# Performance work log

Measured on AMD Instinct MI355X. Metric: run time of the kernel, lower is better.

## Reference

```python
import jax, jax.numpy as jnp
import numpy as np

D = 1024
H = 16
HD = D // H


def setup_inputs() -> dict:
    key = jax.random.key(0)
    ks = jax.random.split(key, 5)
    s = 1.0 / np.sqrt(D)
    return {
        "inputs": jax.random.normal(ks[0], (2, 2048, D), dtype=jnp.float32),
        "Wq": jax.random.normal(ks[1], (D, D), dtype=jnp.float32) * s,
        "bq": jnp.zeros((D,), jnp.float32),
        "Wk": jax.random.normal(ks[2], (D, D), dtype=jnp.float32) * s,
        "bk": jnp.zeros((D,), jnp.float32),
        "Wv": jax.random.normal(ks[3], (D, D), dtype=jnp.float32) * s,
        "bv": jnp.zeros((D,), jnp.float32),
        "Wo": jax.random.normal(ks[4], (D, D), dtype=jnp.float32) * s,
        "bo": jnp.zeros((D,), jnp.float32),
    }


def reference(inputs, Wq, bq, Wk, bk, Wv, bv, Wo, bo):
    B, S, _ = inputs.shape
    def split_heads(x):  # [B,S,D] -> [B,H,S,hd]
        return x.reshape(B, S, H, HD).transpose(0, 2, 1, 3)
    q = split_heads(inputs @ Wq + bq)
    k = split_heads(inputs @ Wk + bk)
    v = split_heads(inputs @ Wv + bv)
    scale = 1.0 / jnp.sqrt(jnp.asarray(HD, inputs.dtype))
    scores = jnp.einsum("bhsd,bhtd->bhst", q, k) * scale  # [B,H,S,S]
    weights = jax.nn.softmax(scores, axis=-1)
    attn = jnp.einsum("bhst,bhtd->bhsd", weights, v)
    concat = attn.transpose(0, 2, 1, 3).reshape(B, S, D)
    return concat @ Wo + bo
```

## Files before the change

kernel.cpp:

```cpp
#include <hip/hip_runtime.h>


typedef __bf16 bf16x8 __attribute__((ext_vector_type(8)));
typedef float  f32x4  __attribute__((ext_vector_type(4)));

#if __has_builtin(__builtin_amdgcn_exp2f)
#define EXPFN(x) __builtin_amdgcn_exp2f(x)
#define QSCALE (0.125f * 1.44269504088896f)
#else
#define EXPFN(x) __expf(x)
#define QSCALE 0.125f
#endif

#define LDKP 74

__device__ __forceinline__ unsigned short f2bf(float f) {
    unsigned int u = __float_as_uint(f);
    u += 0x7FFFu + ((u >> 16) & 1u);
    return (unsigned short)(u >> 16);
}

__device__ __forceinline__ void gload16(const void* g, void* l) {
    __builtin_amdgcn_global_load_lds(
        (const __attribute__((address_space(1))) void*)g,
        (__attribute__((address_space(3))) void*)l, 16, 0, 0);
}

#define WAIT0_BARRIER() asm volatile("s_waitcnt vmcnt(0)\n\ts_barrier" ::: "memory")

__global__ __launch_bounds__(256) void prep_kernel(
    const float* __restrict__ X, ushort4* __restrict__ Xb,
    const float* __restrict__ Wq, const float* __restrict__ Wk,
    const float* __restrict__ Wv, const float* __restrict__ Wo,
    unsigned short* __restrict__ Wt_all) {
    const int z = blockIdx.z;
    if (z == 4) {
        int base = (blockIdx.y * 32 + blockIdx.x) * 1024 + threadIdx.x;
        const float4* X4 = (const float4*)X;
        #pragma unroll
        for (int c = 0; c < 4; c++) {
            int i = base + c * 256;
            float4 v = X4[i];
            ushort4 o;
            o.x = f2bf(v.x); o.y = f2bf(v.y); o.z = f2bf(v.z); o.w = f2bf(v.w);
            Xb[i] = o;
        }
        return;
    }
    __shared__ float tile[32][33];
    const float* W = (z == 0) ? Wq : (z == 1) ? Wk : (z == 2) ? Wv : Wo;
    unsigned short* Wt = Wt_all + (size_t)z * 1024 * 1024;
    int c0 = blockIdx.x * 32, r0 = blockIdx.y * 32;
    int x = threadIdx.x & 31, y = threadIdx.x >> 5;
    for (int j = 0; j < 32; j += 8)
        tile[y + j][x] = W[(r0 + y + j) * 1024 + c0 + x];
    __syncthreads();
    for (int j = 0; j < 32; j += 8)
        Wt[(c0 + y + j) * 1024 + r0 + x] = f2bf(tile[x][y + j]);
}

__global__ __launch_bounds__(256, 2) void gemm_qkv_kernel(
    const unsigned short* __restrict__ Xb, const unsigned short* __restrict__ Wt_all,
    const float* __restrict__ bq, const float* __restrict__ bk,
    const float* __restrict__ bv,
    unsigned short* __restrict__ Qb, unsigned short* __restrict__ Kb,
    unsigned short* __restrict__ Vt) {
    const int x0 = blockIdx.x * 128;
    const int y0 = blockIdx.y * 64;

    __shared__ __align__(16) unsigned short smem[128 * 64 + 3 * 64 * 64];
    unsigned short* As  = smem;
    unsigned short* Bqs = smem + 8192;
    unsigned short* Bks = smem + 12288;
    unsigned short* Bvs = smem + 16384;

    const unsigned short* Ap  = Xb + (size_t)x0 * 1024;
    const unsigned short* Bqp = Wt_all + (size_t)y0 * 1024;
    const unsigned short* Bkp = Wt_all + 1048576u + (size_t)y0 * 1024;
    const unsigned short* Bvp = Wt_all + 2097152u + (size_t)y0 * 1024;

    const int tid = threadIdx.x;
    const int lane = tid & 63, wave = tid >> 6;
    const int quad = lane >> 4, l15 = lane & 15;
    const int wrow = (wave >> 1) * 64, wcol = (wave & 1) * 32;

    f32x4 aq[4][2] = {};
    f32x4 ak[4][2] = {};
    f32x4 av[4][2] = {};

    const int srow = lane >> 3;
    const int ch8  = (lane & 7) * 8;
    const int swz  = (((lane & 7) ^ srow)) * 8;
    const int sw   = (l15 & 7);

    for (int k0 = 0; k0 < 1024; k0 += 64) {
        #pragma unroll
        for (int c = 0; c < 4; c++) {
            int r = c * 32 + wave * 8 + srow;
            gload16(Ap + (size_t)r * 1024 + k0 + swz, &As[r * 64 + ch8]);
        }
        #pragma unroll
        for (int c = 0; c < 2; c++) {
            int r = c * 32 + wave * 8 + srow;
            gload16(Bqp + (size_t)r * 1024 + k0 + swz, &Bqs[r * 64 + ch8]);
            gload16(Bkp + (size_t)r * 1024 + k0 + swz, &Bks[r * 64 + ch8]);
            gload16(Bvp + (size_t)r * 1024 + k0 + swz, &Bvs[r * 64 + ch8]);
        }
        WAIT0_BARRIER();
        #pragma unroll
        for (int kk = 0; kk < 2; kk++) {
            bf16x8 af[4], bqf[2], bkf[2], bvf[2];
            const int co = (((kk * 4 + quad) ^ sw)) * 8;
            #pragma unroll
            for (int i = 0; i < 4; i++)
                af[i] = *(const bf16x8*)&As[(wrow + i * 16 + l15) * 64 + co];
            #pragma unroll
            for (int j = 0; j < 2; j++) {
                bqf[j] = *(const bf16x8*)&Bqs[(wcol + j * 16 + l15) * 64 + co];
                bkf[j] = *(const bf16x8*)&Bks[(wcol + j * 16 + l15) * 64 + co];
                bvf[j] = *(const bf16x8*)&Bvs[(wcol + j * 16 + l15) * 64 + co];
            }
            #pragma unroll
            for (int i = 0; i < 4; i++)
                #pragma unroll
                for (int j = 0; j < 2; j++) {
                    aq[i][j] = __builtin_amdgcn_mfma_f32_16x16x32_bf16(
                        af[i], bqf[j], aq[i][j], 0, 0, 0);
                    ak[i][j] = __builtin_amdgcn_mfma_f32_16x16x32_bf16(
                        af[i], bkf[j], ak[i][j], 0, 0, 0);
                    av[i][j] = __builtin_amdgcn_mfma_f32_16x16x32_bf16(
                        af[i], bvf[j], av[i][j], 0, 0, 0);
                }
        }
        __syncthreads();
    }

    #pragma unroll
    for (int j = 0; j < 2; j++) {
        int col = y0 + wcol + j * 16 + l15;
        float bqc = bq[col], bkc = bk[col];
        int h = col >> 6, d = col & 63;
        #pragma unroll
        for (int i = 0; i < 4; i++)
            #pragma unroll
            for (int r = 0; r < 4; r++) {
                int row = x0 + wrow + i * 16 + quad * 4 + r;
                int b = row >> 11, s = row & 2047;
                size_t idx = (size_t)((b * 16 + h) * 2048 + s) * 64 + d;
                Qb[idx] = f2bf((aq[i][j][r] + bqc) * QSCALE);
                Kb[idx] = f2bf(ak[i][j][r] + bkc);
            }
    }

    __syncthreads();
    unsigned short* vts = smem;
    #pragma unroll
    for (int j = 0; j < 2; j++) {
        int n = wcol + j * 16 + l15;
        float bvc = bv[y0 + n];
        #pragma unroll
        for (int i = 0; i < 4; i++)
            #pragma unroll
            for (int r = 0; r < 4; r++) {
                int m = wrow + i * 16 + quad * 4 + r;
                vts[n * 136 + m] = f2bf(av[i][j][r] + bvc);
            }
    }
    __syncthreads();
    const int bseq = x0 >> 11;
    const int s0 = x0 & 2047;
    #pragma unroll
    for (int q = 0; q < 4; q++) {
        int c = q * 256 + tid;
        int n = c >> 4, mc = c & 15;
        uint4 vv = *(const uint4*)&vts[n * 136 + mc * 8];
        *(uint4*)&Vt[(size_t)(bseq * 1024 + y0 + n) * 2048 + s0 + mc * 8] = vv;
    }
}

__global__ __launch_bounds__(256) void attn_kernel(
    const unsigned short* __restrict__ Qb, const unsigned short* __restrict__ Kb,
    const unsigned short* __restrict__ Vt, unsigned short* __restrict__ Cc,
    float* __restrict__ Op, float* __restrict__ Lp, int tlen, int do_split) {
    const int bh = blockIdx.y;
    const int b = bh >> 4, h = bh & 15;
    const int q0 = blockIdx.x * 128;
    const int split = blockIdx.z;
    const int tbeg = split * tlen;

    const int tid = threadIdx.x;
    const int lane = tid & 63, wave = tid >> 6;
    const int quad = lane >> 4, l15 = lane & 15;

    __shared__ __align__(16) unsigned short Ks[64 * 64];
    __shared__ __align__(16) unsigned short Vs[64 * 64];
    __shared__ __align__(16) unsigned short Ps[4][32 * LDKP];

    const unsigned short* Qbh = Qb + (size_t)bh * 2048 * 64;
    const unsigned short* Kbh = Kb + (size_t)bh * 2048 * 64;
    const unsigned short* Vbh = Vt + (size_t)bh * 64 * 2048;

    bf16x8 qa[2][2];
    #pragma unroll
    for (int mi = 0; mi < 2; mi++)
        #pragma unroll
        for (int kk = 0; kk < 2; kk++)
            qa[mi][kk] = *(const bf16x8*)&Qbh[
                (size_t)(q0 + wave * 32 + mi * 16 + l15) * 64 + kk * 32 + quad * 8];

    union { unsigned short us[8]; bf16x8 v; } ones_u;
    #pragma unroll
    for (int i = 0; i < 8; i++) ones_u.us[i] = 0x3F80;
    const bf16x8 onesv = ones_u.v;

    f32x4 o[2][4] = {};
    f32x4 ol[2] = {};

    const int srow = lane >> 3;
    const int r0s = wave * 16 + srow;
    const int ch8 = (lane & 7) * 8;
    const int swz = (((lane & 7) ^ srow)) * 8;
    const int sw  = (l15 & 7);

    for (int ti = 0; ti < tlen; ti += 64) {
        const int t0 = tbeg + ti;
        __syncthreads();
        gload16(&Kbh[(size_t)(t0 + r0s) * 64 + swz],       &Ks[r0s * 64 + ch8]);
        gload16(&Kbh[(size_t)(t0 + r0s + 8) * 64 + swz],   &Ks[(r0s + 8) * 64 + ch8]);
        gload16(&Vbh[(size_t)r0s * 2048 + t0 + swz],       &Vs[r0s * 64 + ch8]);
        gload16(&Vbh[(size_t)(r0s + 8) * 2048 + t0 + swz], &Vs[(r0s + 8) * 64 + ch8]);
        asm volatile("s_waitcnt vmcnt(0)" ::: "memory");
        __syncthreads();

        f32x4 sf[2][4] = {};
        #pragma unroll
        for (int j = 0; j < 4; j++)
            #pragma unroll
            for (int kk = 0; kk < 2; kk++) {
                bf16x8 kf = *(const bf16x8*)&Ks[(j * 16 + l15) * 64 +
                                                (((kk * 4 + quad) ^ sw)) * 8];
                sf[0][j] = __builtin_amdgcn_mfma_f32_16x16x32_bf16(qa[0][kk], kf, sf[0][j], 0, 0, 0);
                sf[1][j] = __builtin_amdgcn_mfma_f32_16x16x32_bf16(qa[1][kk], kf, sf[1][j], 0, 0, 0);
            }

        #pragma unroll
        for (int mi = 0; mi < 2; mi++)
            #pragma unroll
            for (int j = 0; j < 4; j++)
                #pragma unroll
                for (int r = 0; r < 4; r++) {
                    float p = EXPFN(sf[mi][j][r]);
                    Ps[wave][(mi * 16 + quad * 4 + r) * LDKP + j * 16 + l15] =
                        (unsigned short)(__float_as_uint(p) >> 16);
                }

        asm volatile("s_waitcnt lgkmcnt(0)" ::: "memory");

        #pragma unroll
        for (int kk = 0; kk < 2; kk++) {
            bf16x8 pf0 = *(const bf16x8*)&Ps[wave][(l15) * LDKP + kk * 32 + quad * 8];
            bf16x8 pf1 = *(const bf16x8*)&Ps[wave][(16 + l15) * LDKP + kk * 32 + quad * 8];
            ol[0] = __builtin_amdgcn_mfma_f32_16x16x32_bf16(pf0, onesv, ol[0], 0, 0, 0);
            ol[1] = __builtin_amdgcn_mfma_f32_16x16x32_bf16(pf1, onesv, ol[1], 0, 0, 0);
            #pragma unroll
            for (int j = 0; j < 4; j++) {
                bf16x8 vf = *(const bf16x8*)&Vs[(j * 16 + l15) * 64 +
                                                (((kk * 4 + quad) ^ sw)) * 8];
                o[0][j] = __builtin_amdgcn_mfma_f32_16x16x32_bf16(pf0, vf, o[0][j], 0, 0, 0);
                o[1][j] = __builtin_amdgcn_mfma_f32_16x16x32_bf16(pf1, vf, o[1][j], 0, 0, 0);
            }
        }
    }

    if (do_split) {
        float* Opd = Op + (size_t)(split * 32 + bh) * 2048 * 64;
        float* Lpd = Lp + (size_t)(split * 32 + bh) * 2048;
        #pragma unroll
        for (int mi = 0; mi < 2; mi++)
            #pragma unroll
            for (int r = 0; r < 4; r++) {
                int s = q0 + wave * 32 + mi * 16 + quad * 4 + r;
                if (l15 == 0) Lpd[s] = ol[mi][r];
                #pragma unroll
                for (int j = 0; j < 4; j++)
                    Opd[(size_t)s * 64 + j * 16 + l15] = o[mi][j][r];
            }
    } else {
        #pragma unroll
        for (int mi = 0; mi < 2; mi++)
            #pragma unroll
            for (int r = 0; r < 4; r++) {
                float inv = 1.f / ol[mi][r];
                int s = q0 + wave * 32 + mi * 16 + quad * 4 + r;
                size_t row = (size_t)(b * 2048 + s);
                #pragma unroll
                for (int j = 0; j < 4; j++)
                    Cc[row * 1024 + h * 64 + j * 16 + l15] = f2bf(o[mi][j][r] * inv);
            }
    }
}

__global__ __launch_bounds__(256) void combine_kernel(
    const float4* __restrict__ Op, const float* __restrict__ Lp,
    unsigned short* __restrict__ Cc) {
    int idx = blockIdx.x * 256 + threadIdx.x;
    int d4 = idx & 15;
    int s = (idx >> 4) & 2047;
    int bh = idx >> 15;
    const size_t half4 = (size_t)32 * 2048 * 16;
    float4 a = Op[(size_t)idx], c = Op[half4 + (size_t)idx];
    float l = Lp[bh * 2048 + s] + Lp[32 * 2048 + bh * 2048 + s];
    float inv = 1.f / l;
    ushort4 o;
    o.x = f2bf((a.x + c.x) * inv); o.y = f2bf((a.y + c.y) * inv);
    o.z = f2bf((a.z + c.z) * inv); o.w = f2bf((a.w + c.w) * inv);
    int b = bh >> 4, h = bh & 15;
    *(ushort4*)&Cc[((size_t)(b * 2048 + s)) * 1024 + h * 64 + d4 * 4] = o;
}

__global__ __launch_bounds__(256) void gemm_out_kernel(
    const unsigned short* __restrict__ Cc, const unsigned short* __restrict__ Wot,
    const float* __restrict__ bo, float* __restrict__ out) {
    const int m0 = blockIdx.x * 128;
    const int n0 = blockIdx.y * 64;

    __shared__ __align__(16) unsigned short As[128 * 64];
    __shared__ __align__(16) unsigned short Bs[64 * 64];

    const int tid = threadIdx.x;
    const int lane = tid & 63, wave = tid >> 6;
    const int quad = lane >> 4, l15 = lane & 15;
    const int wrow = (wave >> 1) * 64, wcol = (wave & 1) * 32;

    f32x4 acc[4][2] = {};
    const int srow = lane >> 3;
    const int ch8 = (lane & 7) * 8;
    const int swz = (((lane & 7) ^ srow)) * 8;
    const int sw  = (l15 & 7);

    for (int k0 = 0; k0 < 1024; k0 += 64) {
        #pragma unroll
        for (int c = 0; c < 4; c++) {
            int r = c * 32 + wave * 8 + srow;
            gload16(Cc + (size_t)(m0 + r) * 1024 + k0 + swz, &As[r * 64 + ch8]);
            if (c < 2)
                gload16(Wot + (size_t)(n0 + r) * 1024 + k0 + swz, &Bs[r * 64 + ch8]);
        }
        WAIT0_BARRIER();
        #pragma unroll
        for (int kk = 0; kk < 2; kk++) {
            bf16x8 af[4], bfr[2];
            #pragma unroll
            for (int i = 0; i < 4; i++)
                af[i] = *(const bf16x8*)&As[(wrow + i * 16 + l15) * 64 +
                                            (((kk * 4 + quad) ^ sw)) * 8];
            #pragma unroll
            for (int j = 0; j < 2; j++)
                bfr[j] = *(const bf16x8*)&Bs[(wcol + j * 16 + l15) * 64 +
                                             (((kk * 4 + quad) ^ sw)) * 8];
            #pragma unroll
            for (int i = 0; i < 4; i++)
                #pragma unroll
                for (int j = 0; j < 2; j++)
                    acc[i][j] = __builtin_amdgcn_mfma_f32_16x16x32_bf16(
                        af[i], bfr[j], acc[i][j], 0, 0, 0);
        }
        __syncthreads();
    }

    #pragma unroll
    for (int j = 0; j < 2; j++) {
        int col = n0 + wcol + j * 16 + l15;
        float bcol = bo[col];
        #pragma unroll
        for (int i = 0; i < 4; i++)
            #pragma unroll
            for (int r = 0; r < 4; r++) {
                int row = m0 + wrow + i * 16 + quad * 4 + r;
                out[(size_t)row * 1024 + col] = acc[i][j][r] + bcol;
            }
    }
}

extern "C" void kernel_launch(void* const* d_in, const int* in_sizes, int n_in,
                              void* d_out, int out_size, void* d_ws, size_t ws_size,
                              hipStream_t stream) {
    const float* X  = (const float*)d_in[0];
    const float* Wq = (const float*)d_in[1];
    const float* bq = (const float*)d_in[2];
    const float* Wk = (const float*)d_in[3];
    const float* bk = (const float*)d_in[4];
    const float* Wv = (const float*)d_in[5];
    const float* bv = (const float*)d_in[6];
    const float* Wo = (const float*)d_in[7];
    const float* bo = (const float*)d_in[8];
    float* out = (float*)d_out;

    char* ws = (char*)d_ws;
    unsigned short* Xb = (unsigned short*)(ws);
    unsigned short* Wt = (unsigned short*)(ws + (8u  << 20));
    unsigned short* Qb = (unsigned short*)(ws + (16u << 20));
    unsigned short* Kb = (unsigned short*)(ws + (24u << 20));
    unsigned short* Vt = (unsigned short*)(ws + (32u << 20));
    unsigned short* Cc = (unsigned short*)(ws + (40u << 20));
    float* Op = (float*)(ws + (48u << 20));
    float* Lp = (float*)(ws + (48u << 20) + 33554432u);
    const bool use_split = ws_size >= ((size_t)(48u << 20) + 33554432u + 524288u);

    prep_kernel<<<dim3(32, 32, 5), 256, 0, stream>>>(X, (ushort4*)Xb, Wq, Wk, Wv, Wo, Wt);
    gemm_qkv_kernel<<<dim3(32, 16), 256, 0, stream>>>(Xb, Wt, bq, bk, bv, Qb, Kb, Vt);
    if (use_split) {
        attn_kernel<<<dim3(16, 32, 2), 256, 0, stream>>>(Qb, Kb, Vt, Cc, Op, Lp, 1024, 1);
        combine_kernel<<<4096, 256, 0, stream>>>((const float4*)Op, Lp, Cc);
    } else {
        attn_kernel<<<dim3(16, 32, 1), 256, 0, stream>>>(Qb, Kb, Vt, Cc, Op, Lp, 2048, 0);
    }
    gemm_out_kernel<<<dim3(32, 16), 256, 0, stream>>>(Cc, Wt + 3u * 1024 * 1024, bo, out);
}
```

Before: 190.2 us.

## Double-buffer LDS tiles with async prefetch in QKV, attention and output GEMM kernels

Adds ping-pong shared-memory buffers to the QKV projection, attention and output-projection kernels. The next K-tile (or K/V tile) is issued with global_load_lds before computing on the current one, and partial vmcnt waits replace full drains, so global loads can overlap MFMA work. This doubles LDS use: the QKV GEMM goes to 80KB per block, which may cut its 2-blocks-per-CU occupancy. Correctness depends on the hand-chosen vmcnt counts matching the number of loads issued per stage.

```diff
diff --git a/kernel.cpp b/kernel.cpp
--- a/kernel.cpp
+++ b/kernel.cpp
@@ -14,6 +14,10 @@
 
 #define LDKP 74
 
+#define VMCNT(n)  asm volatile("s_waitcnt vmcnt(" #n ")" ::: "memory")
+#define LGKMCNT0() asm volatile("s_waitcnt lgkmcnt(0)" ::: "memory")
+#define BARRIER() __builtin_amdgcn_s_barrier()
+
 __device__ __forceinline__ unsigned short f2bf(float f) {
     unsigned int u = __float_as_uint(f);
     u += 0x7FFFu + ((u >> 16) & 1u);
@@ -25,8 +29,6 @@
         (const __attribute__((address_space(1))) void*)g,
         (__attribute__((address_space(3))) void*)l, 16, 0, 0);
 }
-
-#define WAIT0_BARRIER() asm volatile("s_waitcnt vmcnt(0)\n\ts_barrier" ::: "memory")
 
 __global__ __launch_bounds__(256) void prep_kernel(
     const float* __restrict__ X, ushort4* __restrict__ Xb,
@@ -68,11 +70,7 @@
     const int x0 = blockIdx.x * 128;
     const int y0 = blockIdx.y * 64;
 
-    __shared__ __align__(16) unsigned short smem[128 * 64 + 3 * 64 * 64];
-    unsigned short* As  = smem;
-    unsigned short* Bqs = smem + 8192;
-    unsigned short* Bks = smem + 12288;
-    unsigned short* Bvs = smem + 16384;
+    __shared__ __align__(16) unsigned short smem[2][20480];
 
     const unsigned short* Ap  = Xb + (size_t)x0 * 1024;
     const unsigned short* Bqp = Wt_all + (size_t)y0 * 1024;
@@ -93,7 +91,11 @@
     const int swz  = (((lane & 7) ^ srow)) * 8;
     const int sw   = (l15 & 7);
 
-    for (int k0 = 0; k0 < 1024; k0 += 64) {
+    auto stage = [&](int buf, int k0) {
+        unsigned short* As  = smem[buf];
+        unsigned short* Bqs = smem[buf] + 8192;
+        unsigned short* Bks = smem[buf] + 12288;
+        unsigned short* Bvs = smem[buf] + 16384;
         #pragma unroll
         for (int c = 0; c < 4; c++) {
             int r = c * 32 + wave * 8 + srow;
@@ -106,7 +108,22 @@
             gload16(Bkp + (size_t)r * 1024 + k0 + swz, &Bks[r * 64 + ch8]);
             gload16(Bvp + (size_t)r * 1024 + k0 + swz, &Bvs[r * 64 + ch8]);
         }
-        WAIT0_BARRIER();
+    };
+
+    stage(0, 0);
+    int cur = 0;
+    for (int k0 = 0; k0 < 1024; k0 += 64) {
+        if (k0 + 64 < 1024) {
+            stage(cur ^ 1, k0 + 64);
+            VMCNT(10);
+        } else {
+            VMCNT(0);
+        }
+        BARRIER();
+        const unsigned short* As  = smem[cur];
+        const unsigned short* Bqs = smem[cur] + 8192;
+        const unsigned short* Bks = smem[cur] + 12288;
+        const unsigned short* Bvs = smem[cur] + 16384;
         #pragma unroll
         for (int kk = 0; kk < 2; kk++) {
             bf16x8 af[4], bqf[2], bkf[2], bvf[2];
@@ -132,7 +149,9 @@
                         af[i], bvf[j], av[i][j], 0, 0, 0);
                 }
         }
-        __syncthreads();
+        LGKMCNT0();
+        BARRIER();
+        cur ^= 1;
     }
 
     #pragma unroll
@@ -152,8 +171,7 @@
             }
     }
 
-    __syncthreads();
-    unsigned short* vts = smem;
+    unsigned short* vts = smem[0];
     #pragma unroll
     for (int j = 0; j < 2; j++) {
         int n = wcol + j * 16 + l15;
@@ -192,8 +210,8 @@
     const int lane = tid & 63, wave = tid >> 6;
     const int quad = lane >> 4, l15 = lane & 15;
 
-    __shared__ __align__(16) unsigned short Ks[64 * 64];
-    __shared__ __align__(16) unsigned short Vs[64 * 64];
+    __shared__ __align__(16) unsigned short Ks[2][64 * 64];
+    __shared__ __align__(16) unsigned short Vs[2][64 * 64];
     __shared__ __align__(16) unsigned short Ps[4][32 * LDKP];
 
     const unsigned short* Qbh = Qb + (size_t)bh * 2048 * 64;
@@ -222,23 +240,33 @@
     const int swz = (((lane & 7) ^ srow)) * 8;
     const int sw  = (l15 & 7);
 
+    auto stage = [&](int buf, int t0) {
+        gload16(&Kbh[(size_t)(t0 + r0s) * 64 + swz],       &Ks[buf][r0s * 64 + ch8]);
+        gload16(&Kbh[(size_t)(t0 + r0s + 8) * 64 + swz],   &Ks[buf][(r0s + 8) * 64 + ch8]);
+        gload16(&Vbh[(size_t)r0s * 2048 + t0 + swz],       &Vs[buf][r0s * 64 + ch8]);
+        gload16(&Vbh[(size_t)(r0s + 8) * 2048 + t0 + swz], &Vs[buf][(r0s + 8) * 64 + ch8]);
+    };
+
+    stage(0, tbeg);
+    int cur = 0;
     for (int ti = 0; ti < tlen; ti += 64) {
-        const int t0 = tbeg + ti;
-        __syncthreads();
-        gload16(&Kbh[(size_t)(t0 + r0s) * 64 + swz],       &Ks[r0s * 64 + ch8]);
-        gload16(&Kbh[(size_t)(t0 + r0s + 8) * 64 + swz],   &Ks[(r0s + 8) * 64 + ch8]);
-        gload16(&Vbh[(size_t)r0s * 2048 + t0 + swz],       &Vs[r0s * 64 + ch8]);
-        gload16(&Vbh[(size_t)(r0s + 8) * 2048 + t0 + swz], &Vs[(r0s + 8) * 64 + ch8]);
-        asm volatile("s_waitcnt vmcnt(0)" ::: "memory");
-        __syncthreads();
+        if (ti + 64 < tlen) {
+            stage(cur ^ 1, tbeg + ti + 64);
+            VMCNT(4);
+        } else {
+            VMCNT(0);
+        }
+        BARRIER();
+        const unsigned short* Ksc = Ks[cur];
+        const unsigned short* Vsc = Vs[cur];
 
         f32x4 sf[2][4] = {};
         #pragma unroll
         for (int j = 0; j < 4; j++)
             #pragma unroll
             for (int kk = 0; kk < 2; kk++) {
-                bf16x8 kf = *(const bf16x8*)&Ks[(j * 16 + l15) * 64 +
-                                                (((kk * 4 + quad) ^ sw)) * 8];
+                bf16x8 kf = *(const bf16x8*)&Ksc[(j * 16 + l15) * 64 +
+                                                 (((kk * 4 + quad) ^ sw)) * 8];
                 sf[0][j] = __builtin_amdgcn_mfma_f32_16x16x32_bf16(qa[0][kk], kf, sf[0][j], 0, 0, 0);
                 sf[1][j] = __builtin_amdgcn_mfma_f32_16x16x32_bf16(qa[1][kk], kf, sf[1][j], 0, 0, 0);
             }
@@ -254,7 +282,7 @@
                         (unsigned short)(__float_as_uint(p) >> 16);
                 }
 
-        asm volatile("s_waitcnt lgkmcnt(0)" ::: "memory");
+        LGKMCNT0();
 
         #pragma unroll
         for (int kk = 0; kk < 2; kk++) {
@@ -264,12 +292,15 @@
             ol[1] = __builtin_amdgcn_mfma_f32_16x16x32_bf16(pf1, onesv, ol[1], 0, 0, 0);
             #pragma unroll
             for (int j = 0; j < 4; j++) {
-                bf16x8 vf = *(const bf16x8*)&Vs[(j * 16 + l15) * 64 +
-                                                (((kk * 4 + quad) ^ sw)) * 8];
+                bf16x8 vf = *(const bf16x8*)&Vsc[(j * 16 + l15) * 64 +
+                                                 (((kk * 4 + quad) ^ sw)) * 8];
                 o[0][j] = __builtin_amdgcn_mfma_f32_16x16x32_bf16(pf0, vf, o[0][j], 0, 0, 0);
                 o[1][j] = __builtin_amdgcn_mfma_f32_16x16x32_bf16(pf1, vf, o[1][j], 0, 0, 0);
             }
         }
+        LGKMCNT0();
+        BARRIER();
+        cur ^= 1;
     }
 
     if (do_split) {
@@ -324,8 +355,8 @@
     const int m0 = blockIdx.x * 128;
     const int n0 = blockIdx.y * 64;
 
-    __shared__ __align__(16) unsigned short As[128 * 64];
-    __shared__ __align__(16) unsigned short Bs[64 * 64];
+    __shared__ __align__(16) unsigned short As[2][128 * 64];
+    __shared__ __align__(16) unsigned short Bs[2][64 * 64];
 
     const int tid = threadIdx.x;
     const int lane = tid & 63, wave = tid >> 6;
@@ -338,26 +369,37 @@
     const int swz = (((lane & 7) ^ srow)) * 8;
     const int sw  = (l15 & 7);
 
-    for (int k0 = 0; k0 < 1024; k0 += 64) {
+    auto stage = [&](int buf, int k0) {
         #pragma unroll
         for (int c = 0; c < 4; c++) {
             int r = c * 32 + wave * 8 + srow;
-            gload16(Cc + (size_t)(m0 + r) * 1024 + k0 + swz, &As[r * 64 + ch8]);
+            gload16(Cc + (size_t)(m0 + r) * 1024 + k0 + swz, &As[buf][r * 64 + ch8]);
             if (c < 2)
-                gload16(Wot + (size_t)(n0 + r) * 1024 + k0 + swz, &Bs[r * 64 + ch8]);
-        }
-        WAIT0_BARRIER();
+                gload16(Wot + (size_t)(n0 + r) * 1024 + k0 + swz, &Bs[buf][r * 64 + ch8]);
+        }
+    };
+
+    stage(0, 0);
+    int cur = 0;
+    for (int k0 = 0; k0 < 1024; k0 += 64) {
+        if (k0 + 64 < 1024) {
+            stage(cur ^ 1, k0 + 64);
+            VMCNT(6);
+        } else {
+            VMCNT(0);
+        }
+        BARRIER();
         #pragma unroll
         for (int kk = 0; kk < 2; kk++) {
             bf16x8 af[4], bfr[2];
             #pragma unroll
             for (int i = 0; i < 4; i++)
-                af[i] = *(const bf16x8*)&As[(wrow + i * 16 + l15) * 64 +
-                                            (((kk * 4 + quad) ^ sw)) * 8];
+                af[i] = *(const bf16x8*)&As[cur][(wrow + i * 16 + l15) * 64 +
+                                                 (((kk * 4 + quad) ^ sw)) * 8];
             #pragma unroll
             for (int j = 0; j < 2; j++)
-                bfr[j] = *(const bf16x8*)&Bs[(wcol + j * 16 + l15) * 64 +
-                                             (((kk * 4 + quad) ^ sw)) * 8];
+                bfr[j] = *(const bf16x8*)&Bs[cur][(wcol + j * 16 + l15) * 64 +
+                                                  (((kk * 4 + quad) ^ sw)) * 8];
             #pragma unroll
             for (int i = 0; i < 4; i++)
                 #pragma unroll
@@ -365,7 +407,9 @@
                     acc[i][j] = __builtin_amdgcn_mfma_f32_16x16x32_bf16(
                         af[i], bfr[j], acc[i][j], 0, 0, 0);
         }
-        __syncthreads();
+        LGKMCNT0();
+        BARRIER();
+        cur ^= 1;
     }
 
     #pragma unroll
```

New measurement: 195.6 us. 2.8% more time.

## Double-buffer K/V tiles and keep softmax probabilities in registers

Applied to the files above, without the earlier changes.

The attention loop now double-buffers the K and V tiles in LDS, so the next tile's async global-to-LDS loads overlap with the current tile's MFMAs. The score MFMA swaps its operands to produce a transposed result, and the K rows are loaded with a permutation, so the exponentiated scores can be packed with v_cvt_pk_bf16_f32 straight into A-operand registers. This removes the per-wave LDS probability buffer and its write/read round trip. In exchange it doubles K/V LDS use and relies on a fragile row-permutation mapping for correctness.

```diff
diff --git a/kernel.cpp b/kernel.cpp
--- a/kernel.cpp
+++ b/kernel.cpp
@@ -12,7 +12,10 @@
 #define QSCALE 0.125f
 #endif
 
-#define LDKP 74
+#define VMCNT(n)  asm volatile("s_waitcnt vmcnt(" #n ")" ::: "memory")
+#define LGKMCNT0() asm volatile("s_waitcnt lgkmcnt(0)" ::: "memory")
+#define BARRIER() __builtin_amdgcn_s_barrier()
+#define WAIT0_BARRIER() asm volatile("s_waitcnt vmcnt(0)\n\ts_barrier" ::: "memory")
 
 __device__ __forceinline__ unsigned short f2bf(float f) {
     unsigned int u = __float_as_uint(f);
@@ -25,8 +28,6 @@
         (const __attribute__((address_space(1))) void*)g,
         (__attribute__((address_space(3))) void*)l, 16, 0, 0);
 }
-
-#define WAIT0_BARRIER() asm volatile("s_waitcnt vmcnt(0)\n\ts_barrier" ::: "memory")
 
 __global__ __launch_bounds__(256) void prep_kernel(
     const float* __restrict__ X, ushort4* __restrict__ Xb,
@@ -192,9 +193,8 @@
     const int lane = tid & 63, wave = tid >> 6;
     const int quad = lane >> 4, l15 = lane & 15;
 
-    __shared__ __align__(16) unsigned short Ks[64 * 64];
-    __shared__ __align__(16) unsigned short Vs[64 * 64];
-    __shared__ __align__(16) unsigned short Ps[4][32 * LDKP];
+    __shared__ __align__(16) unsigned short Ks[2][64 * 64];
+    __shared__ __align__(16) unsigned short Vs[2][64 * 64];
 
     const unsigned short* Qbh = Qb + (size_t)bh * 2048 * 64;
     const unsigned short* Kbh = Kb + (size_t)bh * 2048 * 64;
@@ -222,54 +222,80 @@
     const int swz = (((lane & 7) ^ srow)) * 8;
     const int sw  = (l15 & 7);
 
+    const int pk0 = (r0s & 0x23) | ((r0s & 0x0C) << 1) | ((r0s & 0x10) >> 2);
+    const int r8  = r0s + 8;
+    const int pk8 = (r8 & 0x23) | ((r8 & 0x0C) << 1) | ((r8 & 0x10) >> 2);
+
+    auto stage = [&](int buf, int t0) {
+        gload16(&Kbh[(size_t)(t0 + pk0) * 64 + swz],       &Ks[buf][r0s * 64 + ch8]);
+        gload16(&Kbh[(size_t)(t0 + pk8) * 64 + swz],       &Ks[buf][(r0s + 8) * 64 + ch8]);
+        gload16(&Vbh[(size_t)r0s * 2048 + t0 + swz],       &Vs[buf][r0s * 64 + ch8]);
+        gload16(&Vbh[(size_t)(r0s + 8) * 2048 + t0 + swz], &Vs[buf][(r0s + 8) * 64 + ch8]);
+    };
+
+    stage(0, tbeg);
+    int cur = 0;
     for (int ti = 0; ti < tlen; ti += 64) {
-        const int t0 = tbeg + ti;
-        __syncthreads();
-        gload16(&Kbh[(size_t)(t0 + r0s) * 64 + swz],       &Ks[r0s * 64 + ch8]);
-        gload16(&Kbh[(size_t)(t0 + r0s + 8) * 64 + swz],   &Ks[(r0s + 8) * 64 + ch8]);
-        gload16(&Vbh[(size_t)r0s * 2048 + t0 + swz],       &Vs[r0s * 64 + ch8]);
-        gload16(&Vbh[(size_t)(r0s + 8) * 2048 + t0 + swz], &Vs[(r0s + 8) * 64 + ch8]);
-        asm volatile("s_waitcnt vmcnt(0)" ::: "memory");
-        __syncthreads();
+        if (ti + 64 < tlen) {
+            stage(cur ^ 1, tbeg + ti + 64);
+            VMCNT(4);
+        } else {
+            VMCNT(0);
+        }
+        BARRIER();
+        const unsigned short* Ksc = Ks[cur];
+        const unsigned short* Vsc = Vs[cur];
 
         f32x4 sf[2][4] = {};
         #pragma unroll
         for (int j = 0; j < 4; j++)
             #pragma unroll
             for (int kk = 0; kk < 2; kk++) {
-                bf16x8 kf = *(const bf16x8*)&Ks[(j * 16 + l15) * 64 +
-                                                (((kk * 4 + quad) ^ sw)) * 8];
-                sf[0][j] = __builtin_amdgcn_mfma_f32_16x16x32_bf16(qa[0][kk], kf, sf[0][j], 0, 0, 0);
-                sf[1][j] = __builtin_amdgcn_mfma_f32_16x16x32_bf16(qa[1][kk], kf, sf[1][j], 0, 0, 0);
-            }
-
-        #pragma unroll
-        for (int mi = 0; mi < 2; mi++)
+                bf16x8 kf = *(const bf16x8*)&Ksc[(j * 16 + l15) * 64 +
+                                                 (((kk * 4 + quad) ^ sw)) * 8];
+                sf[0][j] = __builtin_amdgcn_mfma_f32_16x16x32_bf16(kf, qa[0][kk], sf[0][j], 0, 0, 0);
+                sf[1][j] = __builtin_amdgcn_mfma_f32_16x16x32_bf16(kf, qa[1][kk], sf[1][j], 0, 0, 0);
+            }
+
+        union { unsigned int u[4]; bf16x8 v; } pa[2][2];
+        #pragma unroll
+        for (int mi = 0; mi < 2; mi++) {
+            float pe[4][4];
             #pragma unroll
             for (int j = 0; j < 4; j++)
                 #pragma unroll
-                for (int r = 0; r < 4; r++) {
-                    float p = EXPFN(sf[mi][j][r]);
-                    Ps[wave][(mi * 16 + quad * 4 + r) * LDKP + j * 16 + l15] =
-                        (unsigned short)(__float_as_uint(p) >> 16);
+                for (int r = 0; r < 4; r++)
+                    pe[j][r] = EXPFN(sf[mi][j][r]);
+            #pragma unroll
+            for (int kk = 0; kk < 2; kk++)
+                #pragma unroll
+                for (int d = 0; d < 4; d++) {
+                    const int j = 2 * kk + (d >> 1);
+                    const int r = 2 * (d & 1);
+                    unsigned int w;
+                    asm("v_cvt_pk_bf16_f32 %0, %1, %2"
+                        : "=v"(w) : "v"(pe[j][r]), "v"(pe[j][r + 1]));
+                    pa[mi][kk].u[d] = w;
                 }
-
-        asm volatile("s_waitcnt lgkmcnt(0)" ::: "memory");
+        }
 
         #pragma unroll
         for (int kk = 0; kk < 2; kk++) {
-            bf16x8 pf0 = *(const bf16x8*)&Ps[wave][(l15) * LDKP + kk * 32 + quad * 8];
-            bf16x8 pf1 = *(const bf16x8*)&Ps[wave][(16 + l15) * LDKP + kk * 32 + quad * 8];
+            bf16x8 pf0 = pa[0][kk].v;
+            bf16x8 pf1 = pa[1][kk].v;
             ol[0] = __builtin_amdgcn_mfma_f32_16x16x32_bf16(pf0, onesv, ol[0], 0, 0, 0);
             ol[1] = __builtin_amdgcn_mfma_f32_16x16x32_bf16(pf1, onesv, ol[1], 0, 0, 0);
             #pragma unroll
             for (int j = 0; j < 4; j++) {
-                bf16x8 vf = *(const bf16x8*)&Vs[(j * 16 + l15) * 64 +
-                                                (((kk * 4 + quad) ^ sw)) * 8];
+                bf16x8 vf = *(const bf16x8*)&Vsc[(j * 16 + l15) * 64 +
+                                                 (((kk * 4 + quad) ^ sw)) * 8];
                 o[0][j] = __builtin_amdgcn_mfma_f32_16x16x32_bf16(pf0, vf, o[0][j], 0, 0, 0);
                 o[1][j] = __builtin_amdgcn_mfma_f32_16x16x32_bf16(pf1, vf, o[1][j], 0, 0, 0);
             }
         }
+        LGKMCNT0();
+        BARRIER();
+        cur ^= 1;
     }
 
     if (do_split) {
```

Result: faster. 186.1 us (-2.2%).
